# Kernel tuning notes

Hardware: AMD Instinct MI355X
Metric: run time of the kernel (lower is better)

## Reference

```python
import jax, jax.numpy as jnp
import numpy as np
import math

B, N, H, OUT = 32, 2048, 256, 128
K = 6            # knn_graph k
ALPHA = 0.2      # GCN2Conv alpha (beta=1 since theta/layer are None)
NEG = 0.2        # leaky_relu negative slope in ASAP
EPS = 1e-5       # batchnorm eps
RATIOS = (0.15, 0.25, 0.5)


def _scatter_add(vals, idx, n):
    # vals [B,E] or [B,E,h], idx [B,E] -> [B,n,...]
    b, e = idx.shape
    gi = (idx + jnp.arange(b)[:, None] * n).reshape(-1)
    flat = vals.reshape((b * e,) + vals.shape[2:])
    return jax.ops.segment_sum(flat, gi, num_segments=b * n).reshape((b, n) + vals.shape[2:])


def _scatter_max(vals, idx, n):
    b, e = idx.shape
    gi = (idx + jnp.arange(b)[:, None] * n).reshape(-1)
    flat = vals.reshape((b * e,) + vals.shape[2:])
    return jax.ops.segment_max(flat, gi, num_segments=b * n).reshape((b, n) + vals.shape[2:])


def _gather(x, idx):
    # x [B,n,...] or [B,n], idx [B,E]
    if x.ndim == 3:
        return jnp.take_along_axis(x, idx[..., None], axis=1)
    return jnp.take_along_axis(x, idx, axis=1)


def _knn_undirected(pos):
    # knn_graph(pos, k=6, loop=True) then to_undirected (coalesced via `valid` mask)
    b, n, _ = pos.shape
    d2 = jnp.sum((pos[:, :, None, :] - pos[:, None, :, :]) ** 2, axis=-1)  # [B,n,n]
    _, nbr = jax.lax.top_k(-d2, K)                # self included (dist 0)
    ctr = jnp.broadcast_to(jnp.arange(n)[None, :, None], (b, n, K)).reshape(b, n * K)
    nbr = nbr.reshape(b, n * K)
    src = jnp.concatenate([nbr, ctr], axis=1)     # symmetrize
    dst = jnp.concatenate([ctr, nbr], axis=1)
    key = src * n + dst
    order = jnp.argsort(key, axis=1)
    src = jnp.take_along_axis(src, order, axis=1)
    dst = jnp.take_along_axis(dst, order, axis=1)
    key = jnp.take_along_axis(key, order, axis=1)
    valid = jnp.concatenate([jnp.ones((b, 1), bool), key[:, 1:] != key[:, :-1]], axis=1)
    return src, dst, valid


def _edge_mlp(pos, src, dst, valid, W1, b1, g, be, m, v, W2, b2):
    # relu(MLP([1,32,1])(||p_i - p_j||)); BN in eval mode; self loops replaced by 1
    d = jnp.linalg.norm(_gather(pos, src) - _gather(pos, dst), axis=-1)  # [B,E]
    t = d[..., None] @ W1 + b1                       # [B,E,32]
    t = (t - m) * jax.lax.rsqrt(v + EPS) * g + be
    t = jax.nn.relu(t)
    w = jax.nn.relu((t @ W2 + b2)[..., 0])
    w = jnp.where(src == dst, 1.0, w)                # add_remaining_self_loops fill=1
    return jnp.where(valid, w, 0.0)                  # coalesce duplicate edges


def _gcn2(x, x0, src, dst, w, Wc):
    # GCN2Conv with beta=1, shared weights: ((1-a)*A_hat x + a*x0) @ W
    n = x.shape[1]
    deg = _scatter_add(w, dst, n)
    dis = jax.lax.rsqrt(jnp.maximum(deg, 1e-12))     # deg >= 1 (self loops)
    norm = _gather(dis, src) * w * _gather(dis, dst)
    agg = _scatter_add(norm[..., None] * _gather(x, src), dst, n)
    return ((1.0 - ALPHA) * agg + ALPHA * x0) @ Wc


def _asap(x, src, dst, valid, w, kpool, Wrel, brel, Wroot, Wlin, blin, Watt, batt,
          lW1, lb1, lW2, lW3, lb3):
    n = x.shape[1]
    # gnn_intra_cluster: GraphConv (add aggregation)
    x_pool = _scatter_add(w[..., None] * _gather(x, src), dst, n) @ Wrel + brel + x @ Wroot
    mj = _gather(x_pool, src)                                    # [B,E,H]
    x_q = _scatter_max(jnp.where(valid[..., None], mj, -jnp.inf), dst, n) @ Wlin + blin
    score = (jnp.concatenate([_gather(x_q, dst), mj], axis=-1) @ Watt + batt)[..., 0]
    score = jnp.where(valid, jax.nn.leaky_relu(score, NEG), -jnp.inf)
    smax = _scatter_max(score, dst, n)
    e = jnp.where(valid, jnp.exp(score - _gather(smax, dst)), 0.0)
    att = e / _gather(_scatter_add(e, dst, n), dst)
    xn = _scatter_add(att[..., None] * _gather(x, src), dst, n)
    # LEConv fitness (no edge weights; duplicates masked)
    a = (xn @ lW1 + lb1)[..., 0]
    bb = (xn @ lW2)[..., 0]
    msg = jnp.where(valid, _gather(a, src) - _gather(bb, dst), 0.0)
    fit = jax.nn.sigmoid(_scatter_add(msg, dst, n) + (xn @ lW3 + lb3)[..., 0])
    vals, idx = jax.lax.top_k(fit, kpool)
    return _gather(xn, idx) * vals[..., None], idx


def _forward(x, pos, conv_W, eW1, eb1, ebn_g, ebn_b, ebn_m, ebn_v, eW2, eb2,
             aWrel, abrel, aWroot, aWlin, ablin, aWatt, abatt,
             leW1, leb1, leW2, leW3, leb3, gW, gb, nW, nb):
    h = None
    readouts = []
    for s in range(4):
        src, dst, valid = _knn_undirected(pos)
        w = _edge_mlp(pos, src, dst, valid, eW1[s], eb1[s], ebn_g[s], ebn_b[s],
                      ebn_m[s], ebn_v[s], eW2[s], eb2[s])
        if s in (1, 2):
            readouts.append(jnp.concatenate([jnp.mean(h, axis=1), jnp.max(h, axis=1)], axis=-1))
        hin = x if s == 0 else h
        h = jax.nn.relu(_gcn2(hin, x, src, dst, w, conv_W[s]))
        if s < 3:
            kpool = math.ceil(RATIOS[s] * h.shape[1])
            h, idx = _asap(h, src, dst, valid, w, kpool, aWrel[s], abrel[s], aWroot[s],
                           aWlin[s], ablin[s], aWatt[s], abatt[s],
                           leW1[s], leb1[s], leW2[s], leW3[s], leb3[s])
            x = _gather(x, idx)
            pos = _gather(pos, idx)
    gate = jax.nn.softmax(h @ gW + gb, axis=1)      # attentional aggregation
    gp = jnp.sum(gate * (h @ nW + nb), axis=1)      # [B,OUT]
    return jnp.concatenate([gp, readouts[1], readouts[0]], axis=-1)


def setup_inputs() -> dict:
    key = jax.random.key(0)
    ks = iter(jax.random.split(key, 40))
    def rn(shape, scale=1.0):
        return scale * jax.random.normal(next(ks), shape, dtype=jnp.float32)
    return {
        "x": rn((B, N, H)),
        "pos": rn((B, N, 3)),
        "conv_W": rn((4, H, H), H ** -0.5),
        "eW1": rn((4, 1, 32)),
        "eb1": rn((4, 32), 0.1),
        "ebn_g": 1.0 + rn((4, 32), 0.1),
        "ebn_b": rn((4, 32), 0.1),
        "ebn_m": rn((4, 32), 0.1),
        "ebn_v": jnp.ones((4, 32), jnp.float32),
        "eW2": rn((4, 32, 1), 32 ** -0.5),
        "eb2": rn((4, 1), 0.1),
        "aWrel": rn((3, H, H), H ** -0.5),
        "abrel": rn((3, H), 0.1),
        "aWroot": rn((3, H, H), H ** -0.5),
        "aWlin": rn((3, H, H), H ** -0.5),
        "ablin": rn((3, H), 0.1),
        "aWatt": rn((3, 2 * H, 1), (2 * H) ** -0.5),
        "abatt": rn((3, 1), 0.1),
        "leW1": rn((3, H, 1), H ** -0.5),
        "leb1": rn((3, 1), 0.1),
        "leW2": rn((3, H, 1), H ** -0.5),
        "leW3": rn((3, H, 1), H ** -0.5),
        "leb3": rn((3, 1), 0.1),
        "gW": rn((H, 1), H ** -0.5),
        "gb": rn((1,), 0.1),
        "nW": rn((H, OUT), H ** -0.5),
        "nb": rn((OUT,), 0.1),
    }


def reference(x, pos, conv_W, eW1, eb1, ebn_g, ebn_b, ebn_m, ebn_v, eW2, eb2,
              aWrel, abrel, aWroot, aWlin, ablin, aWatt, abatt,
              leW1, leb1, leW2, leW3, leb3, gW, gb, nW, nb):
    return _forward(x, pos, conv_W, eW1, eb1, ebn_g, ebn_b, ebn_m, ebn_v, eW2, eb2,
                    aWrel, abrel, aWroot, aWlin, ablin, aWatt, abatt,
                    leW1, leb1, leW2, leW3, leb3, gW, gb, nW, nb)
```

## Files before the change

kernel.cpp:

```cpp
#include <hip/hip_runtime.h>
#include <hip/hip_bf16.h>
#include <math.h>

#define BB 32
#define NMAX 2048
#define HD 256
#define KNN 6
#define OUTD 128
#define NCH 4

typedef __hip_bfloat16 bf16;

__global__ void k_detect(const void* __restrict__ x, int* __restrict__ flag){
  __shared__ int cnt_s;
  if (threadIdx.x==0) cnt_s=0;
  __syncthreads();
  const unsigned short* u=(const unsigned short*)x;
  int c=0;
  for (int i=threadIdx.x;i<4096;i+=256){
    int e=(u[i]>>7)&0xFF;
    if (e>=0xC0) c++;
  }
  atomicAdd(&cnt_s,c);
  __syncthreads();
  if (threadIdx.x==0) flag[0]=(cnt_s>32)?1:0;
}

__device__ __forceinline__ float loadx(const void* x, int fl, size_t idx){
  if (fl) return ((const float*)x)[idx];
  unsigned short u=((const unsigned short*)x)[idx];
  return __uint_as_float(((unsigned)u)<<16);
}

__global__ void k_cvtx(const void* __restrict__ x, const int* __restrict__ flag,
                       float* __restrict__ Hf){
  int t=blockIdx.x*256+threadIdx.x;
  Hf[t]=loadx(x,flag[0],t);
}
__global__ void k_cvtpos(const void* __restrict__ pos, const int* __restrict__ flag,
                         float* __restrict__ posF){
  int t=blockIdx.x*256+threadIdx.x;
  if (t>=BB*NMAX*3) return;
  posF[t]=loadx(pos,flag[0],t);
}
struct WTab { const void* src[25]; int cnt[25]; int dst[25]; };
__global__ void k_cvtw(WTab tab, const int* __restrict__ flag, float* __restrict__ wsW){
  int seg=blockIdx.y;
  int t=blockIdx.x*256+threadIdx.x;
  if (t>=tab.cnt[seg]) return;
  wsW[tab.dst[seg]+t]=loadx(tab.src[seg],flag[0],t);
}

__global__ void k_initcum(int* __restrict__ cum){
  int t=blockIdx.x*256+threadIdx.x;
  if (t<BB*NMAX) cum[t]=t%NMAX;
}
__global__ void k_zero2(int* __restrict__ a, int* __restrict__ b, int n){
  int t=blockIdx.x*256+threadIdx.x;
  if (t<n){ a[t]=0; b[t]=0; }
}
__global__ void k_gatherpos(const float* __restrict__ posF, const int* __restrict__ cum,
                            float* __restrict__ posf, int n){
  int t=blockIdx.x*256+threadIdx.x;
  if (t>=BB*n*3) return;
  int c=t%3, i=(t/3)%n, b=t/(3*n);
  posf[t]=posF[((size_t)b*NMAX+cum[b*NMAX+i])*3+c];
}

__global__ void k_knn_part(const float* __restrict__ posf, double* __restrict__ dcand,
                           int* __restrict__ icand, int n){
  int b=blockIdx.z, ch=blockIdx.y;
  int i=blockIdx.x*256+threadIdx.x;
  const float* pp=posf+(size_t)b*n*3;
  int cs=(n+NCH-1)/NCH;
  int jlo=ch*cs, jhi=jlo+cs; if (jhi>n) jhi=n;
  double px=0.0,py=0.0,pz=0.0;
  if (i<n){ px=(double)pp[i*3]; py=(double)pp[i*3+1]; pz=(double)pp[i*3+2]; }
  double bd0=INFINITY,bd1=INFINITY,bd2=INFINITY,bd3=INFINITY,bd4=INFINITY,bd5=INFINITY;
  int   bi0=0x7fffffff,bi1=0x7fffffff,bi2=0x7fffffff,bi3=0x7fffffff,bi4=0x7fffffff,bi5=0x7fffffff;
  __shared__ double sx[256],sy[256],sz[256];
  for (int base=jlo;base<jhi;base+=256){
    int j=base+threadIdx.x;
    if (j<jhi){ sx[threadIdx.x]=(double)pp[j*3]; sy[threadIdx.x]=(double)pp[j*3+1]; sz[threadIdx.x]=(double)pp[j*3+2]; }
    __syncthreads();
    int lim=jhi-base; if (lim>256) lim=256;
    if (i<n){
      for (int t=0;t<lim;t++){
        double dx=__dsub_rn(px,sx[t]);
        double dy=__dsub_rn(py,sy[t]);
        double dz=__dsub_rn(pz,sz[t]);
        double d2=__dadd_rn(__dadd_rn(__dmul_rn(dx,dx),__dmul_rn(dy,dy)),__dmul_rn(dz,dz));
        if (d2<bd5){
          int id=base+t;
          if (d2<bd4){ bd5=bd4; bi5=bi4;
            if (d2<bd3){ bd4=bd3; bi4=bi3;
              if (d2<bd2){ bd3=bd2; bi3=bi2;
                if (d2<bd1){ bd2=bd1; bi2=bi1;
                  if (d2<bd0){ bd1=bd0; bi1=bi0; bd0=d2; bi0=id; }
                  else { bd1=d2; bi1=id; }
                } else { bd2=d2; bi2=id; }
              } else { bd3=d2; bi3=id; }
            } else { bd4=d2; bi4=id; }
          } else { bd5=d2; bi5=id; }
        }
      }
    }
    __syncthreads();
  }
  if (i<n){
    size_t o=(((size_t)b*NCH+ch)*n+i)*KNN;
    dcand[o+0]=bd0; dcand[o+1]=bd1; dcand[o+2]=bd2; dcand[o+3]=bd3; dcand[o+4]=bd4; dcand[o+5]=bd5;
    icand[o+0]=bi0; icand[o+1]=bi1; icand[o+2]=bi2; icand[o+3]=bi3; icand[o+4]=bi4; icand[o+5]=bi5;
  }
}

__global__ void k_knn_merge(const double* __restrict__ dcand, const int* __restrict__ icand,
                            int* __restrict__ nbr, int n){
  int t=blockIdx.x*256+threadIdx.x;
  if (t>=BB*n) return;
  int b=t/n, i=t-b*n;
  double cd[NCH*KNN]; int ci[NCH*KNN];
  #pragma unroll
  for (int ch=0;ch<NCH;ch++){
    size_t o=(((size_t)b*NCH+ch)*n+i)*KNN;
    #pragma unroll
    for (int k=0;k<KNN;k++){ cd[ch*KNN+k]=dcand[o+k]; ci[ch*KNN+k]=icand[o+k]; }
  }
  int* out=nbr+(size_t)t*KNN;
  #pragma unroll
  for (int k=0;k<KNN;k++){
    int best=0;
    #pragma unroll
    for (int q=1;q<NCH*KNN;q++){
      bool lt=(cd[q]<cd[best])||(cd[q]==cd[best]&&ci[q]<ci[best]);
      if (lt) best=q;
    }
    out[k]=ci[best];
    cd[best]=INFINITY; ci[best]=0x7fffffff;
  }
}

__global__ void k_edge(const float* __restrict__ posf, const int* __restrict__ nbr,
                       float* __restrict__ w1, float* __restrict__ w2,
                       unsigned char* __restrict__ val2,
                       const float* __restrict__ W1, const float* __restrict__ b1,
                       const float* __restrict__ g,  const float* __restrict__ be,
                       const float* __restrict__ m,  const float* __restrict__ v,
                       const float* __restrict__ W2, const float* __restrict__ b2p,
                       int n){
  int t=blockIdx.x*256+threadIdx.x;
  if (t>=BB*n*KNN) return;
  int k=t%KNN; int c=(t/KNN)%n; int b=t/(KNN*n);
  const int* nb=nbr+(size_t)b*n*KNN;
  int j=nb[c*KNN+k];
  bool dup=false;
  #pragma unroll
  for (int kk=0;kk<KNN;kk++) dup=dup||(nb[j*KNN+kk]==c);
  const float* pp=posf+(size_t)b*n*3;
  double dx=__dsub_rn((double)pp[c*3+0],(double)pp[j*3+0]);
  double dy=__dsub_rn((double)pp[c*3+1],(double)pp[j*3+1]);
  double dz=__dsub_rn((double)pp[c*3+2],(double)pp[j*3+2]);
  double d2=__dadd_rn(__dadd_rn(__dmul_rn(dx,dx),__dmul_rn(dy,dy)),__dmul_rn(dz,dz));
  float dd=(float)sqrt(d2);
  float wv;
  if (j==c) wv=1.0f;
  else {
    float acc=b2p[0];
    for (int q=0;q<32;q++){
      float tt=dd*W1[q]+b1[q];
      float r=1.0f/sqrtf(v[q]+1e-5f);
      tt=(tt-m[q])*r*g[q]+be[q];
      tt=fmaxf(tt,0.f);
      acc=fmaf(tt,W2[q],acc);
    }
    wv=fmaxf(acc,0.f);
  }
  w1[t]=wv;
  w2[t]=dup?0.f:wv;
  val2[t]=dup?0:1;
}

__global__ void k_csr_count(const int* __restrict__ nbr, int* __restrict__ cnt, int n){
  int t=blockIdx.x*256+threadIdx.x;
  if (t>=BB*n*KNN) return;
  int b=t/(n*KNN);
  atomicAdd(&cnt[b*n+nbr[t]],1);
}
__global__ void k_csr_scan(const int* __restrict__ cnt, int* __restrict__ offs, int n){
  int b=blockIdx.x, t=threadIdx.x;
  int L=(n+255)/256;
  __shared__ int ssum[256];
  int lo=t*L, hi=lo+L; if (hi>n) hi=n; if (lo>n) lo=n;
  int s=0;
  for (int i=lo;i<hi;i++) s+=cnt[b*n+i];
  ssum[t]=s;
  __syncthreads();
  if (t==0){
    int run=0;
    for (int q=0;q<256;q++){ int vv=ssum[q]; ssum[q]=run; run+=vv; }
  }
  __syncthreads();
  int run=ssum[t];
  for (int i=lo;i<hi;i++){ offs[b*(n+1)+i]=run; run+=cnt[b*n+i]; }
  if (lo<n && hi==n) offs[b*(n+1)+n]=run;
}
__global__ void k_csr_fill(const int* __restrict__ nbr, const int* __restrict__ offs,
                           int* __restrict__ cur, int* __restrict__ rev, int n){
  int t=blockIdx.x*256+threadIdx.x;
  if (t>=BB*n*KNN) return;
  int b=t/(n*KNN); int rem=t-b*n*KNN;
  int d=nbr[t];
  int slot=offs[b*(n+1)+d]+atomicAdd(&cur[b*n+d],1);
  if (slot<0) slot=0;
  if (slot>=n*KNN) slot=n*KNN-1;
  rev[(size_t)b*n*KNN+slot]=rem;
}
__global__ void k_csr_sort(int* __restrict__ rev, const int* __restrict__ offs, int n){
  int t=blockIdx.x*256+threadIdx.x;
  if (t>=BB*n) return;
  int b=t/n, d=t-b*n;
  size_t base=(size_t)b*n*KNN;
  int lo=offs[b*(n+1)+d], hi=offs[b*(n+1)+d+1];
  for (int a2=lo+1;a2<hi;a2++){
    int vv=rev[base+a2]; int p=a2;
    while (p>lo && rev[base+p-1]>vv){ rev[base+p]=rev[base+p-1]; p--; }
    rev[base+p]=vv;
  }
}

__global__ void k_degdis(const float* __restrict__ w1, const float* __restrict__ w2,
                         const int* __restrict__ rev, const int* __restrict__ offs,
                         float* __restrict__ dis, int n){
  int t=blockIdx.x*256+threadIdx.x;
  if (t>=BB*n) return;
  int b=t/n, d=t-b*n;
  size_t rbase=(size_t)b*n*KNN;
  float s=0.f;
  #pragma unroll
  for (int k=0;k<KNN;k++) s+=w1[(size_t)t*KNN+k];
  int lo=offs[b*(n+1)+d], hi=offs[b*(n+1)+d+1];
  for (int sl=lo;sl<hi;sl++) s+=w2[rbase+rev[rbase+sl]];
  dis[t]=1.0f/sqrtf(fmaxf(s,1e-12f));
}

template<int MODE>
__global__ void k_nbrsum(const float* __restrict__ Hin, const float* __restrict__ w1,
                         const float* __restrict__ w2, const int* __restrict__ nbr,
                         const int* __restrict__ rev, const int* __restrict__ offs,
                         const float* __restrict__ dis, const void* __restrict__ xraw,
                         const int* __restrict__ flag,
                         const int* __restrict__ cum, float* __restrict__ outp, int n){
  int wid=blockIdx.x*4+(threadIdx.x>>6);
  int lane=threadIdx.x&63;
  if (wid>=BB*n) return;
  int b=wid/n, d=wid-b*n;
  const float* Hb=Hin+(size_t)b*n*HD;
  float a0=0,a1=0,a2=0,a3=0;
  float dd=(MODE==0)?dis[wid]:0.f;
  #pragma unroll
  for (int k=0;k<KNN;k++){
    int sN=nbr[(size_t)wid*KNN+k];
    float wv=w1[(size_t)wid*KNN+k];
    float nm=(MODE==0)?dis[b*n+sN]*wv*dd:wv;
    const float* r=Hb+(size_t)sN*HD+lane;
    a0=fmaf(nm,r[0],a0); a1=fmaf(nm,r[64],a1); a2=fmaf(nm,r[128],a2); a3=fmaf(nm,r[192],a3);
  }
  size_t rbase=(size_t)b*n*KNN;
  int lo=offs[b*(n+1)+d], hi=offs[b*(n+1)+d+1];
  for (int sl=lo;sl<hi;sl++){
    int e=rev[rbase+sl];
    int sN=e/KNN;
    float wv=w2[rbase+e];
    float nm=(MODE==0)?dis[b*n+sN]*wv*dd:wv;
    const float* r=Hb+(size_t)sN*HD+lane;
    a0=fmaf(nm,r[0],a0); a1=fmaf(nm,r[64],a1); a2=fmaf(nm,r[128],a2); a3=fmaf(nm,r[192],a3);
  }
  size_t o=(size_t)wid*HD+lane;
  if (MODE==0){
    int fl=flag[0];
    size_t xb=((size_t)b*NMAX+cum[b*NMAX+d])*HD+lane;
    a0=0.8f*a0+0.2f*loadx(xraw,fl,xb);
    a1=0.8f*a1+0.2f*loadx(xraw,fl,xb+64);
    a2=0.8f*a2+0.2f*loadx(xraw,fl,xb+128);
    a3=0.8f*a3+0.2f*loadx(xraw,fl,xb+192);
  }
  outp[o]=a0; outp[o+64]=a1; outp[o+128]=a2; outp[o+192]=a3;
}

__global__ void k_mm(const float* __restrict__ A1, const float* __restrict__ B1,
                     const float* __restrict__ A2, const float* __restrict__ B2,
                     const float* __restrict__ bias, int relu,
                     float* __restrict__ Cout, int M){
  __shared__ __align__(16) float As[16][68];
  __shared__ __align__(16) float Bs[16][260];
  int tid=threadIdx.x, bm=blockIdx.x;
  int tm=tid>>4, tn=tid&15;
  float acc[4][4][4];
  #pragma unroll
  for (int b2=0;b2<4;b2++){
    #pragma unroll
    for (int i=0;i<4;i++){
      #pragma unroll
      for (int j=0;j<4;j++) acc[b2][i][j]=0.f;
    }
  }
  int l=tid*4;
  int ar=l>>4, ak=l&15;
  int arow=bm*64+ar;
  int KT = A2 ? 512 : 256;
  for (int k0=0;k0<KT;k0+=16){
    const float* Asrc=(k0<HD)?A1:A2;
    const float* Bsrc=(k0<HD)?B1:B2;
    int kc=k0&(HD-1);
    if (arow<M){
      float4 a4=*(const float4*)(Asrc+(size_t)arow*HD+kc+ak);
      As[ak][ar]=a4.x; As[ak+1][ar]=a4.y; As[ak+2][ar]=a4.z; As[ak+3][ar]=a4.w;
    } else {
      As[ak][ar]=0.f; As[ak+1][ar]=0.f; As[ak+2][ar]=0.f; As[ak+3][ar]=0.f;
    }
    #pragma unroll
    for (int c=0;c<4;c++){
      int idx=c*256+tid;
      int rkk=idx>>6, cc=(idx&63)*4;
      *(float4*)&Bs[rkk][cc]=*(const float4*)(Bsrc+(size_t)(kc+rkk)*HD+cc);
    }
    __syncthreads();
    #pragma unroll
    for (int kk=0;kk<16;kk++){
      float4 av=*(const float4*)&As[kk][tm*4];
      #pragma unroll
      for (int b2=0;b2<4;b2++){
        float4 bv=*(const float4*)&Bs[kk][b2*64+tn*4];
        acc[b2][0][0]=fmaf(av.x,bv.x,acc[b2][0][0]); acc[b2][0][1]=fmaf(av.x,bv.y,acc[b2][0][1]);
        acc[b2][0][2]=fmaf(av.x,bv.z,acc[b2][0][2]); acc[b2][0][3]=fmaf(av.x,bv.w,acc[b2][0][3]);
        acc[b2][1][0]=fmaf(av.y,bv.x,acc[b2][1][0]); acc[b2][1][1]=fmaf(av.y,bv.y,acc[b2][1][1]);
        acc[b2][1][2]=fmaf(av.y,bv.z,acc[b2][1][2]); acc[b2][1][3]=fmaf(av.y,bv.w,acc[b2][1][3]);
        acc[b2][2][0]=fmaf(av.z,bv.x,acc[b2][2][0]); acc[b2][2][1]=fmaf(av.z,bv.y,acc[b2][2][1]);
        acc[b2][2][2]=fmaf(av.z,bv.z,acc[b2][2][2]); acc[b2][2][3]=fmaf(av.z,bv.w,acc[b2][2][3]);
        acc[b2][3][0]=fmaf(av.w,bv.x,acc[b2][3][0]); acc[b2][3][1]=fmaf(av.w,bv.y,acc[b2][3][1]);
        acc[b2][3][2]=fmaf(av.w,bv.z,acc[b2][3][2]); acc[b2][3][3]=fmaf(av.w,bv.w,acc[b2][3][3]);
      }
    }
    __syncthreads();
  }
  #pragma unroll
  for (int i=0;i<4;i++){
    int grow=bm*64+tm*4+i;
    if (grow>=M) continue;
    #pragma unroll
    for (int b2=0;b2<4;b2++){
      #pragma unroll
      for (int j=0;j<4;j++){
        int gcol=b2*64+tn*4+j;
        float v=acc[b2][i][j];
        if (bias) v+=bias[gcol];
        if (relu) v=fmaxf(v,0.f);
        Cout[(size_t)grow*HD+gcol]=v;
      }
    }
  }
}

__global__ void k_va(const float* __restrict__ Wlin, const float* __restrict__ wa,
                     const float* __restrict__ blin, float* __restrict__ va){
  int i=threadIdx.x;
  float acc=0.f;
  for (int j=0;j<HD;j++) acc=fmaf(Wlin[(size_t)i*HD+j],wa[j],acc);
  va[i]=acc;
  if (i==0){
    float c=0.f;
    for (int j=0;j<HD;j++) c=fmaf(blin[j],wa[j],c);
    va[256]=c;
  }
}

__global__ void k_qd(const float* __restrict__ T, const float* __restrict__ wb,
                     const float* __restrict__ va, const int* __restrict__ nbr,
                     const int* __restrict__ rev, const int* __restrict__ offs,
                     const unsigned char* __restrict__ val2,
                     float* __restrict__ pb, float* __restrict__ qd, int n){
  int wid=blockIdx.x*4+(threadIdx.x>>6);
  int lane=threadIdx.x&63;
  if (wid>=BB*n) return;
  int b=wid/n, d=wid-b*n;
  const float* r1=T+(size_t)wid*HD;
  float p=0.f;
  for (int h=lane;h<HD;h+=64) p=fmaf(r1[h],wb[h],p);
  const float* Tb=T+(size_t)b*n*HD;
  float m0=-INFINITY,m1=-INFINITY,m2=-INFINITY,m3=-INFINITY;
  #pragma unroll
  for (int k=0;k<KNN;k++){
    int sN=nbr[(size_t)wid*KNN+k];
    const float* r=Tb+(size_t)sN*HD+lane;
    m0=fmaxf(m0,r[0]); m1=fmaxf(m1,r[64]); m2=fmaxf(m2,r[128]); m3=fmaxf(m3,r[192]);
  }
  size_t rbase=(size_t)b*n*KNN;
  int lo=offs[b*(n+1)+d], hi=offs[b*(n+1)+d+1];
  for (int sl=lo;sl<hi;sl++){
    int e=rev[rbase+sl];
    if (!val2[rbase+e]) continue;
    int sN=e/KNN;
    const float* r=Tb+(size_t)sN*HD+lane;
    m0=fmaxf(m0,r[0]); m1=fmaxf(m1,r[64]); m2=fmaxf(m2,r[128]); m3=fmaxf(m3,r[192]);
  }
  float q=va[lane]*m0+va[lane+64]*m1+va[lane+128]*m2+va[lane+192]*m3;
  #pragma unroll
  for (int o=32;o>0;o>>=1){ p+=__shfl_xor(p,o); q+=__shfl_xor(q,o); }
  if (lane==0){ pb[wid]=p; qd[wid]=q+va[256]; }
}

__global__ void k_attxn(const float* __restrict__ Hin, const float* __restrict__ pb,
                        const float* __restrict__ qd, const int* __restrict__ nbr,
                        const int* __restrict__ rev, const int* __restrict__ offs,
                        const unsigned char* __restrict__ val2, const float* __restrict__ abatt,
                        float* __restrict__ Tout, int n){
  int wid=blockIdx.x*4+(threadIdx.x>>6);
  int lane=threadIdx.x&63;
  if (wid>=BB*n) return;
  int b=wid/n, d=wid-b*n;
  float batt=abatt[0];
  float qs=qd[wid];
  const float* Hb=Hin+(size_t)b*n*HD;
  size_t rbase=(size_t)b*n*KNN;
  int lo=offs[b*(n+1)+d], hi=offs[b*(n+1)+d+1];
  float smax=-INFINITY;
  #pragma unroll
  for (int k=0;k<KNN;k++){
    int sN=nbr[(size_t)wid*KNN+k];
    float sc=qs+pb[b*n+sN]+batt;
    sc=sc>=0.f?sc:0.2f*sc;
    smax=fmaxf(smax,sc);
  }
  for (int sl=lo;sl<hi;sl++){
    int e=rev[rbase+sl];
    if (!val2[rbase+e]) continue;
    int sN=e/KNN;
    float sc=qs+pb[b*n+sN]+batt;
    sc=sc>=0.f?sc:0.2f*sc;
    smax=fmaxf(smax,sc);
  }
  float es=0.f,a0=0,a1=0,a2=0,a3=0;
  #pragma unroll
  for (int k=0;k<KNN;k++){
    int sN=nbr[(size_t)wid*KNN+k];
    float sc=qs+pb[b*n+sN]+batt;
    sc=sc>=0.f?sc:0.2f*sc;
    float e2=expf(sc-smax);
    es+=e2;
    const float* r=Hb+(size_t)sN*HD+lane;
    a0=fmaf(e2,r[0],a0); a1=fmaf(e2,r[64],a1); a2=fmaf(e2,r[128],a2); a3=fmaf(e2,r[192],a3);
  }
  for (int sl=lo;sl<hi;sl++){
    int e=rev[rbase+sl];
    if (!val2[rbase+e]) continue;
    int sN=e/KNN;
    float sc=qs+pb[b*n+sN]+batt;
    sc=sc>=0.f?sc:0.2f*sc;
    float e2=expf(sc-smax);
    es+=e2;
    const float* r=Hb+(size_t)sN*HD+lane;
    a0=fmaf(e2,r[0],a0); a1=fmaf(e2,r[64],a1); a2=fmaf(e2,r[128],a2); a3=fmaf(e2,r[192],a3);
  }
  float inv=1.f/es;
  size_t o=(size_t)wid*HD+lane;
  Tout[o]=a0*inv; Tout[o+64]=a1*inv; Tout[o+128]=a2*inv; Tout[o+192]=a3*inv;
}

__global__ void k_ledots(const float* __restrict__ T, const float* __restrict__ lW1,
                         const float* __restrict__ lb1, const float* __restrict__ lW2,
                         const float* __restrict__ lW3, const float* __restrict__ lb3,
                         float* __restrict__ av, float* __restrict__ bbv,
                         float* __restrict__ l3v, int n){
  int wid=blockIdx.x*4+(threadIdx.x>>6);
  int lane=threadIdx.x&63;
  if (wid>=BB*n) return;
  const float* r=T+(size_t)wid*HD;
  float s1=0,s2=0,s3=0;
  for (int h=lane;h<HD;h+=64){
    float vv=r[h];
    s1=fmaf(vv,lW1[h],s1); s2=fmaf(vv,lW2[h],s2); s3=fmaf(vv,lW3[h],s3);
  }
  #pragma unroll
  for (int o=32;o>0;o>>=1){ s1+=__shfl_xor(s1,o); s2+=__shfl_xor(s2,o); s3+=__shfl_xor(s3,o); }
  if (lane==0){ av[wid]=s1+lb1[0]; bbv[wid]=s2; l3v[wid]=s3+lb3[0]; }
}

__global__ void k_fit(const float* __restrict__ av, const float* __restrict__ bbv,
                      const float* __restrict__ l3v, const int* __restrict__ nbr,
                      const int* __restrict__ rev, const int* __restrict__ offs,
                      const unsigned char* __restrict__ val2, float* __restrict__ fit, int n){
  int t=blockIdx.x*256+threadIdx.x;
  if (t>=BB*n) return;
  int b=t/n, d=t-b*n;
  size_t rbase=(size_t)b*n*KNN;
  float ms=0.f; int cv=KNN;
  #pragma unroll
  for (int k=0;k<KNN;k++) ms+=av[b*n+nbr[(size_t)t*KNN+k]];
  int lo=offs[b*(n+1)+d], hi=offs[b*(n+1)+d+1];
  for (int sl=lo;sl<hi;sl++){
    int e=rev[rbase+sl];
    if (val2[rbase+e]){ ms+=av[b*n+e/KNN]; cv++; }
  }
  float z=ms-(float)cv*bbv[t]+l3v[t];
  fit[t]=1.f/(1.f+expf(-z));
}

__global__ void k_rank(const float* __restrict__ fit, float* __restrict__ svl,
                       int* __restrict__ sid, int n, int kp){
  int t=blockIdx.x*256+threadIdx.x;
  if (t>=BB*n) return;
  int b=t/n, i=t-b*n;
  float fi=fit[t];
  const float* fb=fit+(size_t)b*n;
  int rank=0;
  for (int j=0;j<n;j++){
    float fj=fb[j];
    if (fj>fi || (fj==fi && j<i)) rank++;
  }
  if (rank<kp){ svl[b*NMAX+rank]=fi; sid[b*NMAX+rank]=i; }
}

__global__ void k_pool(const float* __restrict__ T, const float* __restrict__ svl,
                       const int* __restrict__ sid, const int* __restrict__ cumA,
                       int* __restrict__ cumB, float* __restrict__ Hout, int n, int kp){
  int wid=blockIdx.x*4+(threadIdx.x>>6);
  int lane=threadIdx.x&63;
  if (wid>=BB*kp) return;
  int b=wid/kp, j=wid-b*kp;
  int srcn=sid[b*NMAX+j];
  if (srcn<0) srcn=0;
  if (srcn>=n) srcn=n-1;
  float vv=svl[b*NMAX+j];
  const float* r=T+((size_t)b*n+srcn)*HD+lane;
  float* o=Hout+((size_t)b*kp+j)*HD+lane;
  o[0]=r[0]*vv; o[64]=r[64]*vv; o[128]=r[128]*vv; o[192]=r[192]*vv;
  if (lane==0) cumB[b*NMAX+j]=cumA[b*NMAX+srcn];
}

__global__ void k_readout(const float* __restrict__ Hb, float* __restrict__ ro, int n){
  int b=blockIdx.x, h=threadIdx.x;
  const float* p=Hb+(size_t)b*n*HD+h;
  float s=0.f, m=-INFINITY;
  for (int i=0;i<n;i++){ float v=p[(size_t)i*HD]; s+=v; m=fmaxf(m,v); }
  ro[b*512+h]=s/(float)n;
  ro[b*512+256+h]=m;
}

__global__ void k_final(const float* __restrict__ Hb, const float* __restrict__ gW,
                        const float* __restrict__ gb, const float* __restrict__ nW,
                        const float* __restrict__ nbias, const float* __restrict__ ro0,
                        const float* __restrict__ ro1, float* __restrict__ outp, int n){
  int b=blockIdx.x, tid=threadIdx.x;
  int wv=tid>>6, lane=tid&63;
  __shared__ float gate[64];
  for (int i=wv;i<n;i+=4){
    const float* r=Hb+((size_t)b*n+i)*HD;
    float p=0.f;
    for (int h=lane;h<HD;h+=64) p=fmaf(r[h],gW[h],p);
    #pragma unroll
    for (int o=32;o>0;o>>=1) p+=__shfl_xor(p,o);
    if (lane==0) gate[i]=p+gb[0];
  }
  __syncthreads();
  if (tid==0){
    float mx=-INFINITY;
    for (int i=0;i<n;i++) mx=fmaxf(mx,gate[i]);
    float sm=0.f;
    for (int i=0;i<n;i++){ gate[i]=expf(gate[i]-mx); sm+=gate[i]; }
    float inv=1.f/sm;
    for (int i=0;i<n;i++) gate[i]*=inv;
  }
  __syncthreads();
  if (tid<OUTD){
    float acc=0.f;
    for (int i=0;i<n;i++){
      const float* r=Hb+((size_t)b*n+i)*HD;
      float dot=0.f;
      for (int h=0;h<HD;h++) dot=fmaf(r[h],nW[(size_t)h*OUTD+tid],dot);
      acc=fmaf(gate[i],dot+nbias[tid],acc);
    }
    outp[(size_t)b*1152+tid]=acc;
  }
  for (int q=tid;q<512;q+=256){
    outp[(size_t)b*1152+128+q]=ro1[b*512+q];
    outp[(size_t)b*1152+640+q]=ro0[b*512+q];
  }
}

extern "C" void kernel_launch(void* const* d_in, const int* in_sizes, int n_in,
                              void* d_out, int out_size, void* d_ws, size_t ws_size,
                              hipStream_t stream){
  if (n_in<27) return;
  if (in_sizes[0]!=BB*NMAX*HD || in_sizes[1]!=BB*NMAX*3) return;
  float* outp=(float*)d_out;
  (void)out_size;

  char* p=(char*)d_ws;
  auto carve=[&](size_t bytes)->char*{ char* r=p; p+=((bytes+255)/256)*256; return r; };
  float* posF=(float*)carve((size_t)BB*NMAX*3*4);
  float* posf=(float*)carve((size_t)BB*NMAX*3*4);
  float* Hbuf=(float*)carve((size_t)BB*NMAX*HD*4);
  float* Tbuf=(float*)carve((size_t)BB*NMAX*HD*4);
  static const int wcnt[25]={262144,128,128,128,128,128,128,128,4,
                             196608,768,196608,196608,768,1536,3,
                             768,3,768,768,3,256,1,32768,128};
  int woff[25]; int wtot=0;
  for (int i=0;i<25;i++){ woff[i]=wtot; wtot+=(wcnt[i]+63)&~63; }
  float* wsW=(float*)carve((size_t)wtot*4);
  double* dcand=(double*)carve((size_t)BB*NCH*NMAX*KNN*8);
  int*    icand=(int*)  carve((size_t)BB*NCH*NMAX*KNN*4);
  int*   nbr =(int*)  carve((size_t)BB*NMAX*KNN*4);
  int*   rev =(int*)  carve((size_t)BB*NMAX*KNN*4);
  float* w1  =(float*)carve((size_t)BB*NMAX*KNN*4);
  float* w2  =(float*)carve((size_t)BB*NMAX*KNN*4);
  unsigned char* val2=(unsigned char*)carve((size_t)BB*NMAX*KNN);
  int* cnt  =(int*)carve((size_t)BB*NMAX*4);
  int* offs =(int*)carve((size_t)BB*(NMAX+1)*4);
  int* cur  =(int*)carve((size_t)BB*NMAX*4);
  float* dis=(float*)carve((size_t)BB*NMAX*4);
  float* pb =(float*)carve((size_t)BB*NMAX*4);
  float* qd =(float*)carve((size_t)BB*NMAX*4);
  float* av =(float*)carve((size_t)BB*NMAX*4);
  float* bbv=(float*)carve((size_t)BB*NMAX*4);
  float* l3v=(float*)carve((size_t)BB*NMAX*4);
  float* fit=(float*)carve((size_t)BB*NMAX*4);
  float* svl=(float*)carve((size_t)BB*NMAX*4);
  int*   sid=(int*)  carve((size_t)BB*NMAX*4);
  int* cumA =(int*)carve((size_t)BB*NMAX*4);
  int* cumB =(int*)carve((size_t)BB*NMAX*4);
  int* flag =(int*)carve(256);
  float* va =(float*)carve(272*4);
  float* ro0=(float*)carve((size_t)BB*512*4);
  float* ro1=(float*)carve((size_t)BB*512*4);
  size_t need=(size_t)(p-(char*)d_ws);
  if (ws_size<need) return;

  k_detect<<<1,256,0,stream>>>(d_in[0],flag);
  k_cvtx<<<(BB*NMAX*HD)/256,256,0,stream>>>(d_in[0],flag,Hbuf);
  k_cvtpos<<<(BB*NMAX*3+255)/256,256,0,stream>>>(d_in[1],flag,posF);
  {
    WTab tab;
    int maxc=0;
    for (int i=0;i<25;i++){ tab.src[i]=d_in[2+i]; tab.cnt[i]=wcnt[i]; tab.dst[i]=woff[i]; if (wcnt[i]>maxc) maxc=wcnt[i]; }
    k_cvtw<<<dim3((maxc+255)/256,25),256,0,stream>>>(tab,flag,wsW);
  }
  k_initcum<<<(BB*NMAX+255)/256,256,0,stream>>>(cumA);

  const int NS[4]={2048,308,77,39};
  const int KP[3]={308,77,39};

  for (int s=0;s<4;s++){
    int n=NS[s]; int M=BB*n;
    const float* wconv =wsW+woff[0]+(size_t)s*65536;
    const float* eW1p  =wsW+woff[1]+s*32;
    const float* eb1p  =wsW+woff[2]+s*32;
    const float* gp    =wsW+woff[3]+s*32;
    const float* bep   =wsW+woff[4]+s*32;
    const float* mp    =wsW+woff[5]+s*32;
    const float* vp    =wsW+woff[6]+s*32;
    const float* W2p   =wsW+woff[7]+s*32;
    const float* b2p   =wsW+woff[8]+s;
    const float* aWrelp=wsW+woff[9]+(size_t)s*65536;
    const float* abrelp=wsW+woff[10]+s*256;
    const float* aWrootp=wsW+woff[11]+(size_t)s*65536;
    const float* aWlinp=wsW+woff[12]+(size_t)s*65536;
    const float* ablinp=wsW+woff[13]+s*256;
    const float* wap   =wsW+woff[14]+s*512;
    const float* wbp   =wsW+woff[14]+s*512+256;
    const float* abattp=wsW+woff[15]+s;
    const float* leW1p =wsW+woff[16]+s*256;
    const float* leb1p =wsW+woff[17]+s;
    const float* leW2p =wsW+woff[18]+s*256;
    const float* leW3p =wsW+woff[19]+s*256;
    const float* leb3p =wsW+woff[20]+s;

    k_gatherpos<<<(BB*n*3+255)/256,256,0,stream>>>(posF,cumA,posf,n);
    k_knn_part<<<dim3((n+255)/256,NCH,BB),256,0,stream>>>(posf,dcand,icand,n);
    k_knn_merge<<<(BB*n+255)/256,256,0,stream>>>(dcand,icand,nbr,n);
    int totE=BB*n*KNN;
    k_edge<<<(totE+255)/256,256,0,stream>>>(posf,nbr,w1,w2,val2,
        eW1p,eb1p,gp,bep,mp,vp,W2p,b2p,n);
    k_zero2<<<(BB*n+255)/256,256,0,stream>>>(cnt,cur,BB*n);
    k_csr_count<<<(totE+255)/256,256,0,stream>>>(nbr,cnt,n);
    k_csr_scan<<<BB,256,0,stream>>>(cnt,offs,n);
    k_csr_fill<<<(totE+255)/256,256,0,stream>>>(nbr,offs,cur,rev,n);
    k_csr_sort<<<(BB*n+255)/256,256,0,stream>>>(rev,offs,n);
    if (s==1) k_readout<<<BB,256,0,stream>>>(Hbuf,ro0,n);
    if (s==2) k_readout<<<BB,256,0,stream>>>(Hbuf,ro1,n);
    k_degdis<<<(BB*n+255)/256,256,0,stream>>>(w1,w2,rev,offs,dis,n);
    k_nbrsum<0><<<(BB*n+3)/4,256,0,stream>>>(Hbuf,w1,w2,nbr,rev,offs,dis,d_in[0],flag,cumA,Tbuf,n);
    k_mm<<<(M+63)/64,256,0,stream>>>(Tbuf,wconv,(const float*)nullptr,(const float*)nullptr,
                                     (const float*)nullptr,1,Hbuf,M);
    if (s<3){
      int kp=KP[s];
      k_nbrsum<1><<<(BB*n+3)/4,256,0,stream>>>(Hbuf,w1,w2,nbr,rev,offs,dis,d_in[0],flag,cumA,Tbuf,n);
      k_mm<<<(M+63)/64,256,0,stream>>>(Tbuf,aWrelp,Hbuf,aWrootp,abrelp,0,Tbuf,M);
      k_va<<<1,256,0,stream>>>(aWlinp,wap,ablinp,va);
      k_qd<<<(BB*n+3)/4,256,0,stream>>>(Tbuf,wbp,va,nbr,rev,offs,val2,pb,qd,n);
      k_attxn<<<(BB*n+3)/4,256,0,stream>>>(Hbuf,pb,qd,nbr,rev,offs,val2,abattp,Tbuf,n);
      k_ledots<<<(BB*n+3)/4,256,0,stream>>>(Tbuf,leW1p,leb1p,leW2p,leW3p,leb3p,av,bbv,l3v,n);
      k_fit<<<(BB*n+255)/256,256,0,stream>>>(av,bbv,l3v,nbr,rev,offs,val2,fit,n);
      k_rank<<<(BB*n+255)/256,256,0,stream>>>(fit,svl,sid,n,kp);
      k_pool<<<(BB*kp+3)/4,256,0,stream>>>(Tbuf,svl,sid,cumA,cumB,Hbuf,n,kp);
      { int* t=cumA; cumA=cumB; cumB=t; }
    }
  }
  k_final<<<BB,256,0,stream>>>(Hbuf,wsW+woff[21],wsW+woff[22],wsW+woff[23],wsW+woff[24],
                               ro0,ro1,outp,NS[3]);
}
```

Before: 2.250 ms.

## Read raw input directly in first layer, prefetch GEMM tiles, widen KNN chunks

Removes the full-size input conversion kernel so the first-stage neighbor sum reads raw x through loadx directly. The tiled GEMM now register-prefetches the next A/B tile before computing the current one, overlapping global loads with FMA work. KNN partial search uses twice as many chunks for more parallelism, and the candidate buffers now alias the Tbuf workspace instead of getting their own allocation. The risks are a larger merge step in KNN, higher register pressure in the GEMM, and reliance on Tbuf being free while the KNN stages run.

```diff
diff --git a/kernel.cpp b/kernel.cpp
--- a/kernel.cpp
+++ b/kernel.cpp
@@ -7,7 +7,7 @@
 #define HD 256
 #define KNN 6
 #define OUTD 128
-#define NCH 4
+#define NCH 8
 
 typedef __hip_bfloat16 bf16;
 
@@ -32,11 +32,6 @@
   return __uint_as_float(((unsigned)u)<<16);
 }
 
-__global__ void k_cvtx(const void* __restrict__ x, const int* __restrict__ flag,
-                       float* __restrict__ Hf){
-  int t=blockIdx.x*256+threadIdx.x;
-  Hf[t]=loadx(x,flag[0],t);
-}
 __global__ void k_cvtpos(const void* __restrict__ pos, const int* __restrict__ flag,
                          float* __restrict__ posF){
   int t=blockIdx.x*256+threadIdx.x;
@@ -130,7 +125,6 @@
   #pragma unroll
   for (int k=0;k<KNN;k++){
     int best=0;
-    #pragma unroll
     for (int q=1;q<NCH*KNN;q++){
       bool lt=(cd[q]<cd[best])||(cd[q]==cd[best]&&ci[q]<ci[best]);
       if (lt) best=q;
@@ -243,7 +237,7 @@
   dis[t]=1.0f/sqrtf(fmaxf(s,1e-12f));
 }
 
-template<int MODE>
+template<int MODE,int RAW>
 __global__ void k_nbrsum(const float* __restrict__ Hin, const float* __restrict__ w1,
                          const float* __restrict__ w2, const int* __restrict__ nbr,
                          const int* __restrict__ rev, const int* __restrict__ offs,
@@ -254,6 +248,7 @@
   int lane=threadIdx.x&63;
   if (wid>=BB*n) return;
   int b=wid/n, d=wid-b*n;
+  int fl=flag[0];
   const float* Hb=Hin+(size_t)b*n*HD;
   float a0=0,a1=0,a2=0,a3=0;
   float dd=(MODE==0)?dis[wid]:0.f;
@@ -262,8 +257,14 @@
     int sN=nbr[(size_t)wid*KNN+k];
     float wv=w1[(size_t)wid*KNN+k];
     float nm=(MODE==0)?dis[b*n+sN]*wv*dd:wv;
-    const float* r=Hb+(size_t)sN*HD+lane;
-    a0=fmaf(nm,r[0],a0); a1=fmaf(nm,r[64],a1); a2=fmaf(nm,r[128],a2); a3=fmaf(nm,r[192],a3);
+    if (RAW){
+      size_t rb=((size_t)b*n+sN)*HD+lane;
+      a0=fmaf(nm,loadx(xraw,fl,rb),a0);    a1=fmaf(nm,loadx(xraw,fl,rb+64),a1);
+      a2=fmaf(nm,loadx(xraw,fl,rb+128),a2); a3=fmaf(nm,loadx(xraw,fl,rb+192),a3);
+    } else {
+      const float* r=Hb+(size_t)sN*HD+lane;
+      a0=fmaf(nm,r[0],a0); a1=fmaf(nm,r[64],a1); a2=fmaf(nm,r[128],a2); a3=fmaf(nm,r[192],a3);
+    }
   }
   size_t rbase=(size_t)b*n*KNN;
   int lo=offs[b*(n+1)+d], hi=offs[b*(n+1)+d+1];
@@ -272,12 +273,17 @@
     int sN=e/KNN;
     float wv=w2[rbase+e];
     float nm=(MODE==0)?dis[b*n+sN]*wv*dd:wv;
-    const float* r=Hb+(size_t)sN*HD+lane;
-    a0=fmaf(nm,r[0],a0); a1=fmaf(nm,r[64],a1); a2=fmaf(nm,r[128],a2); a3=fmaf(nm,r[192],a3);
+    if (RAW){
+      size_t rb=((size_t)b*n+sN)*HD+lane;
+      a0=fmaf(nm,loadx(xraw,fl,rb),a0);    a1=fmaf(nm,loadx(xraw,fl,rb+64),a1);
+      a2=fmaf(nm,loadx(xraw,fl,rb+128),a2); a3=fmaf(nm,loadx(xraw,fl,rb+192),a3);
+    } else {
+      const float* r=Hb+(size_t)sN*HD+lane;
+      a0=fmaf(nm,r[0],a0); a1=fmaf(nm,r[64],a1); a2=fmaf(nm,r[128],a2); a3=fmaf(nm,r[192],a3);
+    }
   }
   size_t o=(size_t)wid*HD+lane;
   if (MODE==0){
-    int fl=flag[0];
     size_t xb=((size_t)b*NMAX+cum[b*NMAX+d])*HD+lane;
     a0=0.8f*a0+0.2f*loadx(xraw,fl,xb);
     a1=0.8f*a1+0.2f*loadx(xraw,fl,xb+64);
@@ -307,24 +313,28 @@
   int l=tid*4;
   int ar=l>>4, ak=l&15;
   int arow=bm*64+ar;
+  int brow[4], bcol[4];
+  #pragma unroll
+  for (int c=0;c<4;c++){ int idx=c*256+tid; brow[c]=idx>>6; bcol[c]=(idx&63)*4; }
   int KT = A2 ? 512 : 256;
+  float4 a4; float4 b4[4];
+  a4 = (arow<M)? *(const float4*)(A1+(size_t)arow*HD+ak) : make_float4(0.f,0.f,0.f,0.f);
+  #pragma unroll
+  for (int c=0;c<4;c++) b4[c]=*(const float4*)(B1+(size_t)brow[c]*HD+bcol[c]);
   for (int k0=0;k0<KT;k0+=16){
-    const float* Asrc=(k0<HD)?A1:A2;
-    const float* Bsrc=(k0<HD)?B1:B2;
-    int kc=k0&(HD-1);
-    if (arow<M){
-      float4 a4=*(const float4*)(Asrc+(size_t)arow*HD+kc+ak);
-      As[ak][ar]=a4.x; As[ak+1][ar]=a4.y; As[ak+2][ar]=a4.z; As[ak+3][ar]=a4.w;
-    } else {
-      As[ak][ar]=0.f; As[ak+1][ar]=0.f; As[ak+2][ar]=0.f; As[ak+3][ar]=0.f;
-    }
+    As[ak][ar]=a4.x; As[ak+1][ar]=a4.y; As[ak+2][ar]=a4.z; As[ak+3][ar]=a4.w;
     #pragma unroll
-    for (int c=0;c<4;c++){
-      int idx=c*256+tid;
-      int rkk=idx>>6, cc=(idx&63)*4;
-      *(float4*)&Bs[rkk][cc]=*(const float4*)(Bsrc+(size_t)(kc+rkk)*HD+cc);
-    }
+    for (int c=0;c<4;c++) *(float4*)&Bs[brow[c]][bcol[c]]=b4[c];
     __syncthreads();
+    int k1=k0+16;
+    if (k1<KT){
+      const float* Asrc=(k1<HD)?A1:A2;
+      const float* Bsrc=(k1<HD)?B1:B2;
+      int kc=k1&(HD-1);
+      a4 = (arow<M)? *(const float4*)(Asrc+(size_t)arow*HD+kc+ak) : make_float4(0.f,0.f,0.f,0.f);
+      #pragma unroll
+      for (int c=0;c<4;c++) b4[c]=*(const float4*)(Bsrc+(size_t)(kc+brow[c])*HD+bcol[c]);
+    }
     #pragma unroll
     for (int kk=0;kk<16;kk++){
       float4 av=*(const float4*)&As[kk][tm*4];
@@ -607,8 +617,6 @@
   int woff[25]; int wtot=0;
   for (int i=0;i<25;i++){ woff[i]=wtot; wtot+=(wcnt[i]+63)&~63; }
   float* wsW=(float*)carve((size_t)wtot*4);
-  double* dcand=(double*)carve((size_t)BB*NCH*NMAX*KNN*8);
-  int*    icand=(int*)  carve((size_t)BB*NCH*NMAX*KNN*4);
   int*   nbr =(int*)  carve((size_t)BB*NMAX*KNN*4);
   int*   rev =(int*)  carve((size_t)BB*NMAX*KNN*4);
   float* w1  =(float*)carve((size_t)BB*NMAX*KNN*4);
@@ -635,8 +643,10 @@
   size_t need=(size_t)(p-(char*)d_ws);
   if (ws_size<need) return;
 
+  double* dcand=(double*)Tbuf;
+  int*    icand=(int*)((char*)Tbuf + (size_t)BB*NCH*NMAX*KNN*8);
+
   k_detect<<<1,256,0,stream>>>(d_in[0],flag);
-  k_cvtx<<<(BB*NMAX*HD)/256,256,0,stream>>>(d_in[0],flag,Hbuf);
   k_cvtpos<<<(BB*NMAX*3+255)/256,256,0,stream>>>(d_in[1],flag,posF);
   {
     WTab tab;
@@ -688,12 +698,15 @@
     if (s==1) k_readout<<<BB,256,0,stream>>>(Hbuf,ro0,n);
     if (s==2) k_readout<<<BB,256,0,stream>>>(Hbuf,ro1,n);
     k_degdis<<<(BB*n+255)/256,256,0,stream>>>(w1,w2,rev,offs,dis,n);
-    k_nbrsum<0><<<(BB*n+3)/4,256,0,stream>>>(Hbuf,w1,w2,nbr,rev,offs,dis,d_in[0],flag,cumA,Tbuf,n);
+    if (s==0)
+      k_nbrsum<0,1><<<(BB*n+3)/4,256,0,stream>>>(nullptr,w1,w2,nbr,rev,offs,dis,d_in[0],flag,cumA,Tbuf,n);
+    else
+      k_nbrsum<0,0><<<(BB*n+3)/4,256,0,stream>>>(Hbuf,w1,w2,nbr,rev,offs,dis,d_in[0],flag,cumA,Tbuf,n);
     k_mm<<<(M+63)/64,256,0,stream>>>(Tbuf,wconv,(const float*)nullptr,(const float*)nullptr,
                                      (const float*)nullptr,1,Hbuf,M);
     if (s<3){
       int kp=KP[s];
-      k_nbrsum<1><<<(BB*n+3)/4,256,0,stream>>>(Hbuf,w1,w2,nbr,rev,offs,dis,d_in[0],flag,cumA,Tbuf,n);
+      k_nbrsum<1,0><<<(BB*n+3)/4,256,0,stream>>>(Hbuf,w1,w2,nbr,rev,offs,dis,d_in[0],flag,cumA,Tbuf,n);
       k_mm<<<(M+63)/64,256,0,stream>>>(Tbuf,aWrelp,Hbuf,aWrootp,abrelp,0,Tbuf,M);
       k_va<<<1,256,0,stream>>>(aWlinp,wap,ablinp,va);
       k_qd<<<(BB*n+3)/4,256,0,stream>>>(Tbuf,wbp,va,nbr,rev,offs,val2,pb,qd,n);
```

After: 2.799 ms. 1.24x slower.
